# Optimization experiments

Hardware: AMD Instinct MI355X
Metric: run time of the kernel (lower is better)

Reference implementation:

```python
import jax, jax.numpy as jnp
import numpy as np

B, LVS, WIDTH, DEPTH = 8192, 512, 512, 7
EPS = 1e-5
SLOPE = 0.01  # torch LeakyReLU default negative_slope


def setup_inputs() -> dict:
    key = jax.random.key(0)
    ks = jax.random.split(key, 16)
    inp = {"x": jax.random.normal(ks[0], (B, LVS), dtype=jnp.float32)}
    for i in range(DEPTH):
        fan_in = LVS + WIDTH * i
        inp[f"W{i}"] = jax.random.normal(ks[1 + i], (WIDTH, fan_in), dtype=jnp.float32) / np.sqrt(fan_in)
    inp["b"] = 0.01 * jax.random.normal(ks[8], (DEPTH, WIDTH), dtype=jnp.float32)
    inp["gamma"] = jnp.ones((DEPTH, WIDTH), dtype=jnp.float32)
    inp["beta"] = jnp.zeros((DEPTH, WIDTH), dtype=jnp.float32)
    cin = LVS + DEPTH * WIDTH  # 4096
    inp["Wc"] = jax.random.normal(ks[9], (1, cin), dtype=jnp.float32) / np.sqrt(cin)
    inp["bc"] = jnp.zeros((1,), dtype=jnp.float32)
    # torch: rv = randn(...) * 0.02 + 1, multiplied onto each projection
    inp["noise"] = 1.0 + 0.02 * jax.random.normal(ks[10], (DEPTH, B, WIDTH), dtype=jnp.float32)
    return inp


def reference(x, W0, W1, W2, W3, W4, W5, W6, b, gamma, beta, Wc, bc, noise):
    Ws = (W0, W1, W2, W3, W4, W5, W6)
    last = x
    for i in range(DEPTH):
        # Linear: [B, in_i] @ [in_i, width]
        h = jnp.einsum('bi,wi->bw', last, Ws[i]) + b[i]
        # BatchNorm1d (training mode: batch stats, biased variance)
        mean = jnp.mean(h, axis=0)
        var = jnp.mean(jnp.square(h - mean), axis=0)
        h = (h - mean) * jax.lax.rsqrt(var + EPS) * gamma[i] + beta[i]
        # LeakyReLU + multiplicative noise, fused elementwise
        h = jnp.where(h >= 0, h, SLOPE * h) * noise[i]
        last = jnp.concatenate((last, h), axis=-1)
    logits = jnp.einsum('bi,oi->bo', last, Wc) + bc
    return jax.nn.sigmoid(logits)
```

## Files before the change

kernel.cpp:

```cpp
#include <hip/hip_runtime.h>

#define B_ROWS 8192
#define WIDTH  512
#define DEPTH  7
#define CIN    4096
#define EPS    1e-5f
#define SLOPE  0.01f

typedef __attribute__((ext_vector_type(8))) short short8;
typedef __attribute__((ext_vector_type(4))) short short4v;
typedef __attribute__((ext_vector_type(4))) float f32x4;
typedef __attribute__((ext_vector_type(16))) float f32x16;

__device__ inline short f2bf(float f) {
  unsigned u = __builtin_bit_cast(unsigned, f);
  unsigned r = (u + 0x7FFFu + ((u >> 16) & 1u)) >> 16;
  return (short)r;
}

__device__ inline void gl_lds16(const void* g, void* l) {
  __builtin_amdgcn_global_load_lds(
      (const __attribute__((address_space(1))) unsigned*)g,
      (__attribute__((address_space(3))) unsigned*)l, 16, 0, 0);
}

struct WP { const float* p[7]; };

__global__ __launch_bounds__(256) void convw(WP wp, short* __restrict__ out) {
  long e = ((long)blockIdx.x * 256 + threadIdx.x) * 4;
  int layer; long base;
  if      (e < 262144L)  { layer = 0; base = 0; }
  else if (e < 786432L)  { layer = 1; base = 262144L; }
  else if (e < 1572864L) { layer = 2; base = 786432L; }
  else if (e < 2621440L) { layer = 3; base = 1572864L; }
  else if (e < 3932160L) { layer = 4; base = 2621440L; }
  else if (e < 5505024L) { layer = 5; base = 3932160L; }
  else                   { layer = 6; base = 5505024L; }
  f32x4 v = *(const f32x4*)(wp.p[layer] + (e - base));
  short4v o;
  o.x = f2bf(v.x); o.y = f2bf(v.y); o.z = f2bf(v.z); o.w = f2bf(v.w);
  *(short4v*)(out + e) = o;
}

__global__ __launch_bounds__(256) void initx(const float* __restrict__ x,
                                             const float* __restrict__ wc,
                                             short* __restrict__ lastbf,
                                             float* __restrict__ logit,
                                             float* __restrict__ sumsz) {
  int gid = blockIdx.x * 256 + threadIdx.x;
  if (gid < DEPTH * 1024) sumsz[gid] = 0.f;
  int w = threadIdx.x >> 6, l = threadIdx.x & 63;
  int r = blockIdx.x * 4 + w;
  const float* xr = x + (long)r * 512 + l * 8;
  f32x4 v0 = *(const f32x4*)xr;
  f32x4 v1 = *(const f32x4*)(xr + 4);
  const float* wcr = wc + l * 8;
  float acc = 0.f;
  short8 ob;
#pragma unroll
  for (int j = 0; j < 4; ++j) { acc += v0[j] * wcr[j];     ob[j]     = f2bf(v0[j]); }
#pragma unroll
  for (int j = 0; j < 4; ++j) { acc += v1[j] * wcr[4 + j]; ob[4 + j] = f2bf(v1[j]); }
  *(short8*)&lastbf[(long)r * CIN + l * 8] = ob;
#pragma unroll
  for (int off = 32; off; off >>= 1) acc += __shfl_xor(acc, off);
  if (l == 0) logit[r] = acc;
}

__global__ __launch_bounds__(256, 2) void gemm_fused(const short* __restrict__ A,
                                                     const short* __restrict__ Bw,
                                                     float* __restrict__ C,
                                                     float* __restrict__ sums,
                                                     int K) {
  __shared__ __align__(16) char smem[49152];
  int t = threadIdx.x;
  int ks = t >> 6, l = t & 63;
  int l31 = l & 31, hi = l >> 5;
  int bm = blockIdx.x, bn = blockIdx.y;
  const short* Ab = A + (long)(bm * 128) * CIN;
  const short* Bb = Bw + (long)(bn * 64) * K;

  f32x16 acc[4][2];
#pragma unroll
  for (int m = 0; m < 4; ++m)
#pragma unroll
    for (int n = 0; n < 2; ++n)
#pragma unroll
      for (int r = 0; r < 16; ++r) acc[m][n][r] = 0.f;

  int l8 = l >> 3;
  int scol = ((l & 7) ^ l8) << 3;

#define STAGE(buf, k0)                                                                       \
  {                                                                                          \
    char* base = smem + (buf) * 24576;                                                       \
    int c0 = ks * 4, c1 = ks * 2;                                                            \
    gl_lds16(Ab + (long)((c0    ) * 8 + l8) * CIN + (k0) + scol, base + (c0    ) * 1024);    \
    gl_lds16(Ab + (long)((c0 + 1) * 8 + l8) * CIN + (k0) + scol, base + (c0 + 1) * 1024);    \
    gl_lds16(Ab + (long)((c0 + 2) * 8 + l8) * CIN + (k0) + scol, base + (c0 + 2) * 1024);    \
    gl_lds16(Ab + (long)((c0 + 3) * 8 + l8) * CIN + (k0) + scol, base + (c0 + 3) * 1024);    \
    gl_lds16(Bb + (long)((c1    ) * 8 + l8) * K + (k0) + scol, base + 16384 + (c1    ) * 1024); \
    gl_lds16(Bb + (long)((c1 + 1) * 8 + l8) * K + (k0) + scol, base + 16384 + (c1 + 1) * 1024); \
  }

  STAGE(0, 0);
  __syncthreads();

  int kb = ks * 32 + hi * 16;
  int sw = (l & 7) << 4;

  int nt = K >> 6;
  int cur = 0;
  for (int tix = 0; tix < nt; ++tix) {
    if (tix + 1 < nt) STAGE(cur ^ 1, (tix + 1) << 6);
    const char* AsC = smem + cur * 24576;
    const char* BsC = AsC + 16384;
    short8 a[4], b[2];
#pragma unroll
    for (int m = 0; m < 4; ++m)
      a[m] = *(const short8*)(AsC + (m * 32 + l31) * 128 + (kb ^ sw));
#pragma unroll
    for (int n = 0; n < 2; ++n)
      b[n] = *(const short8*)(BsC + (n * 32 + l31) * 128 + (kb ^ sw));
#pragma unroll
    for (int m = 0; m < 4; ++m)
#pragma unroll
      for (int n = 0; n < 2; ++n)
        acc[m][n] = __builtin_amdgcn_mfma_f32_32x32x16_bf16(a[m], b[n], acc[m][n], 0, 0, 0);
    __syncthreads();
    cur ^= 1;
  }

  float* Red = (float*)smem;
#define RIDX(m, n, r) (((m) * 32 + ((r) & 3) + 8 * ((r) >> 2) + 4 * hi) * 64 + (n) * 32 + l31)
  if (ks == 3) {
#pragma unroll
    for (int m = 0; m < 4; ++m)
#pragma unroll
      for (int n = 0; n < 2; ++n)
#pragma unroll
        for (int r = 0; r < 16; ++r) Red[RIDX(m, n, r)] = acc[m][n][r];
  }
  __syncthreads();
  if (ks == 2) {
#pragma unroll
    for (int m = 0; m < 4; ++m)
#pragma unroll
      for (int n = 0; n < 2; ++n)
#pragma unroll
        for (int r = 0; r < 16; ++r) Red[RIDX(m, n, r)] += acc[m][n][r];
  }
  __syncthreads();
  if (ks == 1) {
#pragma unroll
    for (int m = 0; m < 4; ++m)
#pragma unroll
      for (int n = 0; n < 2; ++n)
#pragma unroll
        for (int r = 0; r < 16; ++r) Red[RIDX(m, n, r)] += acc[m][n][r];
  }
  __syncthreads();
  if (ks == 0) {
    float* Cb = C + (long)(bm * 128) * WIDTH + bn * 64;
#pragma unroll
    for (int n = 0; n < 2; ++n) {
      float s = 0.f, q = 0.f;
#pragma unroll
      for (int m = 0; m < 4; ++m) {
#pragma unroll
        for (int r = 0; r < 16; ++r) {
          int cr = (r & 3) + 8 * (r >> 2) + 4 * hi;
          float v = acc[m][n][r] + Red[RIDX(m, n, r)];
          Cb[(long)(m * 32 + cr) * WIDTH + n * 32 + l31] = v;
          s += v; q += v * v;
        }
      }
      s += __shfl_xor(s, 32);
      q += __shfl_xor(q, 32);
      if (l < 32) {
        int colg = bn * 64 + n * 32 + l;
        atomicAdd(&sums[colg], s);
        atomicAdd(&sums[WIDTH + colg], q);
      }
    }
  }
#undef RIDX
#undef STAGE
}

__global__ __launch_bounds__(256) void bnact(const float* __restrict__ h,
                                             const float* __restrict__ sums,
                                             const float* __restrict__ gamma,
                                             const float* __restrict__ beta,
                                             const float* __restrict__ noise,
                                             const float* __restrict__ wc,
                                             short* __restrict__ lastseg,
                                             float* __restrict__ logit) {
  int w = threadIdx.x >> 6, l = threadIdx.x & 63;
  int r = blockIdx.x * 4 + w;
  int c = l * 8;
  const float invB = 1.0f / 8192.0f;
  f32x4 h0 = *(const f32x4*)&h[(long)r * WIDTH + c];
  f32x4 h1 = *(const f32x4*)&h[(long)r * WIDTH + c + 4];
  f32x4 n0 = *(const f32x4*)&noise[(long)r * WIDTH + c];
  f32x4 n1 = *(const f32x4*)&noise[(long)r * WIDTH + c + 4];
  float acc = 0.f;
  short8 ob;
#pragma unroll
  for (int j = 0; j < 8; ++j) {
    int cc = c + j;
    float hv = j < 4 ? h0[j] : h1[j - 4];
    float nv = j < 4 ? n0[j] : n1[j - 4];
    float mean = sums[cc] * invB;
    float var = sums[WIDTH + cc] * invB - mean * mean;
    float v = (hv - mean) * rsqrtf(var + EPS);
    v = v * gamma[cc] + beta[cc];
    v = v >= 0.f ? v : SLOPE * v;
    v *= nv;
    acc += v * wc[cc];
    ob[j] = f2bf(v);
  }
  *(short8*)&lastseg[(long)r * CIN + c] = ob;
#pragma unroll
  for (int off = 32; off; off >>= 1) acc += __shfl_xor(acc, off);
  if (l == 0) logit[r] += acc;
}

__global__ __launch_bounds__(256) void finalize(const float* __restrict__ logit,
                                                const float* __restrict__ bc,
                                                float* __restrict__ out) {
  int i = blockIdx.x * 256 + threadIdx.x;
  float z = logit[i] + bc[0];
  out[i] = 1.0f / (1.0f + expf(-z));
}

extern "C" void kernel_launch(void* const* d_in, const int* in_sizes, int n_in,
                              void* d_out, int out_size, void* d_ws, size_t ws_size,
                              hipStream_t stream) {
  (void)in_sizes; (void)n_in; (void)out_size; (void)ws_size;
  const float* x     = (const float*)d_in[0];
  WP wp;
  for (int i = 0; i < 7; ++i) wp.p[i] = (const float*)d_in[1 + i];
  const float* gamma = (const float*)d_in[9];
  const float* beta  = (const float*)d_in[10];
  const float* Wc    = (const float*)d_in[11];
  const float* bc    = (const float*)d_in[12];
  const float* noise = (const float*)d_in[13];

  char* ws = (char*)d_ws;
  short* lastbf = (short*)ws;
  float* hpre   = (float*)(ws + 67108864);
  short* wbf    = (short*)(ws + 67108864 + 16777216);
  float* sums   = (float*)(ws + 67108864 + 16777216 + 14680064);
  float* logit  = (float*)(ws + 67108864 + 16777216 + 14680064 + 28672);

  convw<<<7168, 256, 0, stream>>>(wp, wbf);
  initx<<<2048, 256, 0, stream>>>(x, Wc, lastbf, logit, sums);

  long woff = 0;
  for (int i = 0; i < DEPTH; ++i) {
    int K = 512 * (i + 1);
    gemm_fused<<<dim3(64, 8), 256, 0, stream>>>(lastbf, wbf + woff, hpre,
                                                sums + i * 1024, K);
    bnact<<<2048, 256, 0, stream>>>(hpre, sums + i * 1024,
                                    gamma + i * 512, beta + i * 512,
                                    noise + (long)i * B_ROWS * WIDTH,
                                    Wc + 512 + i * 512,
                                    lastbf + 512 + (long)i * 512, logit);
    woff += (long)512 * K;
  }
  finalize<<<32, 256, 0, stream>>>(logit, bc, (float*)d_out);
}
```

Baseline: 287.9 us.

## Triple-buffer GEMM LDS pipeline with vmcnt waits and split-K reduction tree

Moves the fused GEMM from double to triple buffering in LDS. Loads are issued two tiles ahead, and full __syncthreads are replaced with explicit s_waitcnt vmcnt plus s_barrier, so global_load_lds traffic overlaps MFMA work. MFMA sections get raised wave priority via s_setprio. The split-K reduction across the four waves drops from three serialized barrier stages to two by using a second reduction buffer. The cost is 72KB of LDS per block, which may stop two blocks fitting per CU under launch_bounds(256,2).

Result: slower. 304.0 us (+5.6%).

```diff
diff --git a/kernel.cpp b/kernel.cpp
--- a/kernel.cpp
+++ b/kernel.cpp
@@ -72,7 +72,7 @@
                                                      float* __restrict__ C,
                                                      float* __restrict__ sums,
                                                      int K) {
-  __shared__ __align__(16) char smem[49152];
+  __shared__ __align__(16) char smem[73728];
   int t = threadIdx.x;
   int ks = t >> 6, l = t & 63;
   int l31 = l & 31, hi = l >> 5;
@@ -90,56 +90,87 @@
 
   int l8 = l >> 3;
   int scol = ((l & 7) ^ l8) << 3;
-
-#define STAGE(buf, k0)                                                                       \
-  {                                                                                          \
-    char* base = smem + (buf) * 24576;                                                       \
-    int c0 = ks * 4, c1 = ks * 2;                                                            \
-    gl_lds16(Ab + (long)((c0    ) * 8 + l8) * CIN + (k0) + scol, base + (c0    ) * 1024);    \
-    gl_lds16(Ab + (long)((c0 + 1) * 8 + l8) * CIN + (k0) + scol, base + (c0 + 1) * 1024);    \
-    gl_lds16(Ab + (long)((c0 + 2) * 8 + l8) * CIN + (k0) + scol, base + (c0 + 2) * 1024);    \
-    gl_lds16(Ab + (long)((c0 + 3) * 8 + l8) * CIN + (k0) + scol, base + (c0 + 3) * 1024);    \
-    gl_lds16(Bb + (long)((c1    ) * 8 + l8) * K + (k0) + scol, base + 16384 + (c1    ) * 1024); \
-    gl_lds16(Bb + (long)((c1 + 1) * 8 + l8) * K + (k0) + scol, base + 16384 + (c1 + 1) * 1024); \
-  }
-
-  STAGE(0, 0);
-  __syncthreads();
+  const short* pA0 = Ab + (long)((ks * 4 + 0) * 8 + l8) * CIN + scol;
+  const short* pA1 = Ab + (long)((ks * 4 + 1) * 8 + l8) * CIN + scol;
+  const short* pA2 = Ab + (long)((ks * 4 + 2) * 8 + l8) * CIN + scol;
+  const short* pA3 = Ab + (long)((ks * 4 + 3) * 8 + l8) * CIN + scol;
+  const short* pB0 = Bb + (long)((ks * 2 + 0) * 8 + l8) * K + scol;
+  const short* pB1 = Bb + (long)((ks * 2 + 1) * 8 + l8) * K + scol;
+
+#define STAGE(base, k0)                                       \
+  {                                                           \
+    gl_lds16(pA0 + (k0), (base) + (ks * 4 + 0) * 1024);       \
+    gl_lds16(pA1 + (k0), (base) + (ks * 4 + 1) * 1024);       \
+    gl_lds16(pA2 + (k0), (base) + (ks * 4 + 2) * 1024);       \
+    gl_lds16(pA3 + (k0), (base) + (ks * 4 + 3) * 1024);       \
+    gl_lds16(pB0 + (k0), (base) + 16384 + (ks * 2 + 0) * 1024); \
+    gl_lds16(pB1 + (k0), (base) + 16384 + (ks * 2 + 1) * 1024); \
+  }
 
   int kb = ks * 32 + hi * 16;
   int sw = (l & 7) << 4;
 
+#define KITER(rb, sb, do_stage, k2, vmlit)                                     \
+  {                                                                            \
+    if (do_stage) STAGE((sb), (k2));                                           \
+    const char* AsC = (rb);                                                    \
+    const char* BsC = (rb) + 16384;                                            \
+    short8 a[4], b[2];                                                         \
+    _Pragma("unroll")                                                          \
+    for (int m = 0; m < 4; ++m)                                                \
+      a[m] = *(const short8*)(AsC + (m * 32 + l31) * 128 + (kb ^ sw));         \
+    _Pragma("unroll")                                                          \
+    for (int n = 0; n < 2; ++n)                                                \
+      b[n] = *(const short8*)(BsC + (n * 32 + l31) * 128 + (kb ^ sw));         \
+    __builtin_amdgcn_s_setprio(1);                                             \
+    _Pragma("unroll")                                                          \
+    for (int m = 0; m < 4; ++m)                                                \
+      _Pragma("unroll")                                                        \
+      for (int n = 0; n < 2; ++n)                                              \
+        acc[m][n] = __builtin_amdgcn_mfma_f32_32x32x16_bf16(a[m], b[n],        \
+                                                            acc[m][n], 0, 0, 0); \
+    __builtin_amdgcn_s_setprio(0);                                             \
+    asm volatile("s_waitcnt vmcnt(" #vmlit ")" ::: "memory");                  \
+    __builtin_amdgcn_s_barrier();                                              \
+  }
+
+  char* buf0 = smem;
+  char* buf1 = smem + 24576;
+  char* buf2 = smem + 49152;
+
+  STAGE(buf0, 0);
+  STAGE(buf1, 64);
+  asm volatile("s_waitcnt vmcnt(6)" ::: "memory");
+  __builtin_amdgcn_s_barrier();
+
   int nt = K >> 6;
-  int cur = 0;
-  for (int tix = 0; tix < nt; ++tix) {
-    if (tix + 1 < nt) STAGE(cur ^ 1, (tix + 1) << 6);
-    const char* AsC = smem + cur * 24576;
-    const char* BsC = AsC + 16384;
-    short8 a[4], b[2];
+  int tix = 0;
+  for (; tix < nt - 2; ++tix) {
+    KITER(buf0, buf2, true, ((tix + 2) << 6), 6);
+    char* tmp = buf0; buf0 = buf1; buf1 = buf2; buf2 = tmp;
+  }
+  KITER(buf0, buf2, false, 0, 0);
+  { char* tmp = buf0; buf0 = buf1; buf1 = buf2; buf2 = tmp; }
+  KITER(buf0, buf2, false, 0, 0);
+
+  float* Red0 = (float*)smem;
+  float* Red1 = (float*)(smem + 32768);
+#define RIDX(m, n, r) (((m) * 32 + ((r) & 3) + 8 * ((r) >> 2) + 4 * hi) * 64 + (n) * 32 + l31)
+  if (ks == 1) {
 #pragma unroll
     for (int m = 0; m < 4; ++m)
-      a[m] = *(const short8*)(AsC + (m * 32 + l31) * 128 + (kb ^ sw));
-#pragma unroll
-    for (int n = 0; n < 2; ++n)
-      b[n] = *(const short8*)(BsC + (n * 32 + l31) * 128 + (kb ^ sw));
+#pragma unroll
+      for (int n = 0; n < 2; ++n)
+#pragma unroll
+        for (int r = 0; r < 16; ++r) Red0[RIDX(m, n, r)] = acc[m][n][r];
+  }
+  if (ks == 3) {
 #pragma unroll
     for (int m = 0; m < 4; ++m)
 #pragma unroll
       for (int n = 0; n < 2; ++n)
-        acc[m][n] = __builtin_amdgcn_mfma_f32_32x32x16_bf16(a[m], b[n], acc[m][n], 0, 0, 0);
-    __syncthreads();
-    cur ^= 1;
-  }
-
-  float* Red = (float*)smem;
-#define RIDX(m, n, r) (((m) * 32 + ((r) & 3) + 8 * ((r) >> 2) + 4 * hi) * 64 + (n) * 32 + l31)
-  if (ks == 3) {
-#pragma unroll
-    for (int m = 0; m < 4; ++m)
-#pragma unroll
-      for (int n = 0; n < 2; ++n)
-#pragma unroll
-        for (int r = 0; r < 16; ++r) Red[RIDX(m, n, r)] = acc[m][n][r];
+#pragma unroll
+        for (int r = 0; r < 16; ++r) Red1[RIDX(m, n, r)] = acc[m][n][r];
   }
   __syncthreads();
   if (ks == 2) {
@@ -148,16 +179,10 @@
 #pragma unroll
       for (int n = 0; n < 2; ++n)
 #pragma unroll
-        for (int r = 0; r < 16; ++r) Red[RIDX(m, n, r)] += acc[m][n][r];
-  }
-  __syncthreads();
-  if (ks == 1) {
-#pragma unroll
-    for (int m = 0; m < 4; ++m)
-#pragma unroll
-      for (int n = 0; n < 2; ++n)
-#pragma unroll
-        for (int r = 0; r < 16; ++r) Red[RIDX(m, n, r)] += acc[m][n][r];
+        for (int r = 0; r < 16; ++r) {
+          float v = acc[m][n][r] + Red1[RIDX(m, n, r)];
+          Red1[RIDX(m, n, r)] = v;
+        }
   }
   __syncthreads();
   if (ks == 0) {
@@ -170,7 +195,7 @@
 #pragma unroll
         for (int r = 0; r < 16; ++r) {
           int cr = (r & 3) + 8 * (r >> 2) + 4 * hi;
-          float v = acc[m][n][r] + Red[RIDX(m, n, r)];
+          float v = acc[m][n][r] + Red0[RIDX(m, n, r)] + Red1[RIDX(m, n, r)];
           Cb[(long)(m * 32 + cr) * WIDTH + n * 32 + l31] = v;
           s += v; q += v * v;
         }
@@ -185,6 +210,7 @@
     }
   }
 #undef RIDX
+#undef KITER
 #undef STAGE
 }
 
```

## Shrink GEMM tile to 64x64, double grid, and parallelize split-K reduction

Applied to the files above, without the earlier changes.

Halves the M tile of the fused GEMM from 128 to 64 rows, doubling the grid to 1024 blocks and raising the occupancy hint to 4 blocks per CU with smaller LDS. The split-K reduction now has two warps write to separate LDS buffers at once, cutting one barrier stage. Pointer setup for the async loads is hoisted out of the loop. The intent is better CU fill on a 256-CU part, at the cost of less reuse per block and more B-matrix traffic.

After: 308.6 us. 1.07x slower.

```diff
diff --git a/kernel.cpp b/kernel.cpp
--- a/kernel.cpp
+++ b/kernel.cpp
@@ -67,22 +67,22 @@
   if (l == 0) logit[r] = acc;
 }
 
-__global__ __launch_bounds__(256, 2) void gemm_fused(const short* __restrict__ A,
+__global__ __launch_bounds__(256, 4) void gemm_fused(const short* __restrict__ A,
                                                      const short* __restrict__ Bw,
                                                      float* __restrict__ C,
                                                      float* __restrict__ sums,
                                                      int K) {
-  __shared__ __align__(16) char smem[49152];
+  __shared__ __align__(16) char smem[32768];
   int t = threadIdx.x;
   int ks = t >> 6, l = t & 63;
   int l31 = l & 31, hi = l >> 5;
   int bm = blockIdx.x, bn = blockIdx.y;
-  const short* Ab = A + (long)(bm * 128) * CIN;
+  const short* Ab = A + (long)(bm * 64) * CIN;
   const short* Bb = Bw + (long)(bn * 64) * K;
 
-  f32x16 acc[4][2];
-#pragma unroll
-  for (int m = 0; m < 4; ++m)
+  f32x16 acc[2][2];
+#pragma unroll
+  for (int m = 0; m < 2; ++m)
 #pragma unroll
     for (int n = 0; n < 2; ++n)
 #pragma unroll
@@ -90,20 +90,20 @@
 
   int l8 = l >> 3;
   int scol = ((l & 7) ^ l8) << 3;
-
-#define STAGE(buf, k0)                                                                       \
-  {                                                                                          \
-    char* base = smem + (buf) * 24576;                                                       \
-    int c0 = ks * 4, c1 = ks * 2;                                                            \
-    gl_lds16(Ab + (long)((c0    ) * 8 + l8) * CIN + (k0) + scol, base + (c0    ) * 1024);    \
-    gl_lds16(Ab + (long)((c0 + 1) * 8 + l8) * CIN + (k0) + scol, base + (c0 + 1) * 1024);    \
-    gl_lds16(Ab + (long)((c0 + 2) * 8 + l8) * CIN + (k0) + scol, base + (c0 + 2) * 1024);    \
-    gl_lds16(Ab + (long)((c0 + 3) * 8 + l8) * CIN + (k0) + scol, base + (c0 + 3) * 1024);    \
-    gl_lds16(Bb + (long)((c1    ) * 8 + l8) * K + (k0) + scol, base + 16384 + (c1    ) * 1024); \
-    gl_lds16(Bb + (long)((c1 + 1) * 8 + l8) * K + (k0) + scol, base + 16384 + (c1 + 1) * 1024); \
-  }
-
-  STAGE(0, 0);
+  const short* pA0 = Ab + (long)((ks * 2 + 0) * 8 + l8) * CIN + scol;
+  const short* pA1 = Ab + (long)((ks * 2 + 1) * 8 + l8) * CIN + scol;
+  const short* pB0 = Bb + (long)((ks * 2 + 0) * 8 + l8) * K + scol;
+  const short* pB1 = Bb + (long)((ks * 2 + 1) * 8 + l8) * K + scol;
+
+#define STAGE(base, k0)                                         \
+  {                                                             \
+    gl_lds16(pA0 + (k0), (base) + (ks * 2 + 0) * 1024);         \
+    gl_lds16(pA1 + (k0), (base) + (ks * 2 + 1) * 1024);         \
+    gl_lds16(pB0 + (k0), (base) + 8192 + (ks * 2 + 0) * 1024);  \
+    gl_lds16(pB1 + (k0), (base) + 8192 + (ks * 2 + 1) * 1024);  \
+  }
+
+  STAGE(smem, 0);
   __syncthreads();
 
   int kb = ks * 32 + hi * 16;
@@ -112,18 +112,18 @@
   int nt = K >> 6;
   int cur = 0;
   for (int tix = 0; tix < nt; ++tix) {
-    if (tix + 1 < nt) STAGE(cur ^ 1, (tix + 1) << 6);
-    const char* AsC = smem + cur * 24576;
-    const char* BsC = AsC + 16384;
-    short8 a[4], b[2];
-#pragma unroll
-    for (int m = 0; m < 4; ++m)
+    if (tix + 1 < nt) STAGE(smem + (cur ^ 1) * 16384, (tix + 1) << 6);
+    const char* AsC = smem + cur * 16384;
+    const char* BsC = AsC + 8192;
+    short8 a[2], b[2];
+#pragma unroll
+    for (int m = 0; m < 2; ++m)
       a[m] = *(const short8*)(AsC + (m * 32 + l31) * 128 + (kb ^ sw));
 #pragma unroll
     for (int n = 0; n < 2; ++n)
       b[n] = *(const short8*)(BsC + (n * 32 + l31) * 128 + (kb ^ sw));
 #pragma unroll
-    for (int m = 0; m < 4; ++m)
+    for (int m = 0; m < 2; ++m)
 #pragma unroll
       for (int n = 0; n < 2; ++n)
         acc[m][n] = __builtin_amdgcn_mfma_f32_32x32x16_bf16(a[m], b[n], acc[m][n], 0, 0, 0);
@@ -131,46 +131,46 @@
     cur ^= 1;
   }
 
-  float* Red = (float*)smem;
+  float* Red0 = (float*)smem;
+  float* Red1 = (float*)(smem + 16384);
 #define RIDX(m, n, r) (((m) * 32 + ((r) & 3) + 8 * ((r) >> 2) + 4 * hi) * 64 + (n) * 32 + l31)
+  if (ks == 1) {
+#pragma unroll
+    for (int m = 0; m < 2; ++m)
+#pragma unroll
+      for (int n = 0; n < 2; ++n)
+#pragma unroll
+        for (int r = 0; r < 16; ++r) Red0[RIDX(m, n, r)] = acc[m][n][r];
+  }
   if (ks == 3) {
 #pragma unroll
-    for (int m = 0; m < 4; ++m)
-#pragma unroll
-      for (int n = 0; n < 2; ++n)
-#pragma unroll
-        for (int r = 0; r < 16; ++r) Red[RIDX(m, n, r)] = acc[m][n][r];
+    for (int m = 0; m < 2; ++m)
+#pragma unroll
+      for (int n = 0; n < 2; ++n)
+#pragma unroll
+        for (int r = 0; r < 16; ++r) Red1[RIDX(m, n, r)] = acc[m][n][r];
   }
   __syncthreads();
   if (ks == 2) {
 #pragma unroll
-    for (int m = 0; m < 4; ++m)
-#pragma unroll
-      for (int n = 0; n < 2; ++n)
-#pragma unroll
-        for (int r = 0; r < 16; ++r) Red[RIDX(m, n, r)] += acc[m][n][r];
-  }
-  __syncthreads();
-  if (ks == 1) {
-#pragma unroll
-    for (int m = 0; m < 4; ++m)
-#pragma unroll
-      for (int n = 0; n < 2; ++n)
-#pragma unroll
-        for (int r = 0; r < 16; ++r) Red[RIDX(m, n, r)] += acc[m][n][r];
+    for (int m = 0; m < 2; ++m)
+#pragma unroll
+      for (int n = 0; n < 2; ++n)
+#pragma unroll
+        for (int r = 0; r < 16; ++r) Red1[RIDX(m, n, r)] += acc[m][n][r];
   }
   __syncthreads();
   if (ks == 0) {
-    float* Cb = C + (long)(bm * 128) * WIDTH + bn * 64;
+    float* Cb = C + (long)(bm * 64) * WIDTH + bn * 64;
 #pragma unroll
     for (int n = 0; n < 2; ++n) {
       float s = 0.f, q = 0.f;
 #pragma unroll
-      for (int m = 0; m < 4; ++m) {
+      for (int m = 0; m < 2; ++m) {
 #pragma unroll
         for (int r = 0; r < 16; ++r) {
           int cr = (r & 3) + 8 * (r >> 2) + 4 * hi;
-          float v = acc[m][n][r] + Red[RIDX(m, n, r)];
+          float v = acc[m][n][r] + Red0[RIDX(m, n, r)] + Red1[RIDX(m, n, r)];
           Cb[(long)(m * 32 + cr) * WIDTH + n * 32 + l31] = v;
           s += v; q += v * v;
         }
@@ -260,8 +260,8 @@
   long woff = 0;
   for (int i = 0; i < DEPTH; ++i) {
     int K = 512 * (i + 1);
-    gemm_fused<<<dim3(64, 8), 256, 0, stream>>>(lastbf, wbf + woff, hpre,
-                                                sums + i * 1024, K);
+    gemm_fused<<<dim3(128, 8), 256, 0, stream>>>(lastbf, wbf + woff, hpre,
+                                                 sums + i * 1024, K);
     bnact<<<2048, 256, 0, stream>>>(hpre, sums + i * 1024,
                                     gamma + i * 512, beta + i * 512,
                                     noise + (long)i * B_ROWS * WIDTH,
```
